# Kernel optimization log

Hardware: AMD Instinct MI355X
Metric: run time of the kernel (lower is better)

The kernel has to match this reference:

```python
import jax, jax.numpy as jnp
import numpy as np

HEADS = 20
HEAD_DIM = 64
NUM_TOKENS = 4


def _split_heads(x, B):
    # (B, S, H*D) -> (B, H, S, D)
    return x.reshape(B, -1, HEADS, HEAD_DIM).transpose(0, 2, 1, 3)


def setup_inputs() -> dict:
    key = jax.random.key(0)
    ks = jax.random.split(key, 10)
    B, HW, hid, cad, Ltxt = 2, 4096, 1280, 2048, 77
    w = lambda k, shp: (jax.random.normal(k, shp, jnp.float32) * 0.02)
    return {
        "hidden_states": jax.random.normal(ks[0], (B, HW, hid), jnp.float32),
        "encoder_hidden_states": jax.random.normal(ks[1], (B, Ltxt + NUM_TOKENS, cad), jnp.float32),
        "indices_to_alter": jax.random.randint(ks[2], (B,), 0, Ltxt, jnp.int32),
        "Wq": w(ks[3], (hid, hid)),
        "Wk": w(ks[4], (cad, hid)),
        "Wv": w(ks[5], (cad, hid)),
        "Wk_nest": w(ks[6], (cad, hid)),
        "Wv_nest": w(ks[7], (cad, hid)),
        "Wout": w(ks[8], (hid, hid)),
        "b_out": jnp.zeros((hid,), jnp.float32),
    }


def reference(hidden_states, encoder_hidden_states, indices_to_alter,
              Wq, Wk, Wv, Wk_nest, Wv_nest, Wout, b_out):
    B, HW, _ = hidden_states.shape
    end = encoder_hidden_states.shape[1] - NUM_TOKENS
    txt = encoder_hidden_states[:, :end]   # (B, Ltxt, cad)
    img = encoder_hidden_states[:, end:]   # (B, num_tokens, cad)

    q = _split_heads(hidden_states @ Wq, B)   # (B, H, HW, D)
    k = _split_heads(txt @ Wk, B)             # (B, H, Lt, D)
    v = _split_heads(txt @ Wv, B)             # (B, H, Lt, D)
    kn = _split_heads(img @ Wk_nest, B)       # (B, H, T, D)
    vn = _split_heads(img @ Wv_nest, B)       # (B, H, T, D)

    sc = 1.0 / jnp.sqrt(jnp.float32(HEAD_DIM))

    # nested attention: per-spatial-position identity value V* (SDPA over image tokens)
    wn = jax.nn.softmax(jnp.einsum('bhqd,bhkd->bhqk', q, kn) * sc, axis=-1)
    value_id = jnp.einsum('bhqk,bhkd->bhqd', wn, vn)          # (B, H, HW, D)

    # main cross attention over text tokens
    w = jax.nn.softmax(jnp.einsum('bhqd,bhkd->bhqk', q, k) * sc, axis=-1)  # (B,H,HW,Lt)
    base = jnp.einsum('bhqk,bhkd->bhqd', w, v)                # (B, H, HW, D)

    # V_mixed[b,h,i] differs from value only at text slot s_b, where it equals value_id[b,h,i].
    # sum_k w[...,k] * V_mixed[...,k,:] == w @ v + w[...,s]*(value_id - v[:, :, s])
    s = indices_to_alter
    w_s = jnp.take_along_axis(w, s[:, None, None, None], axis=3)   # (B, H, HW, 1)
    v_s = jnp.take_along_axis(v, s[:, None, None, None], axis=2)   # (B, H, 1, D)
    out = base + w_s * (value_id - v_s)                             # (B, H, HW, D)

    out = out.transpose(0, 2, 1, 3).reshape(B, HW, HEADS * HEAD_DIM)
    return out @ Wout + b_out
```

## Files before the change

### kernel.cpp

```cpp
#include <hip/hip_runtime.h>
#include <hip/hip_bf16.h>


typedef unsigned short ushort_t;
typedef __attribute__((ext_vector_type(8))) short short8;
typedef __attribute__((ext_vector_type(4))) float f32x4;

#define B_   2
#define HW_  4096
#define HID_ 1280
#define CAD_ 2048
#define LTXT 77
#define NTOK 4
#define NH_  20
#define HD_  64

__device__ __forceinline__ ushort_t f2bf(float f) {
    __hip_bfloat16 h = __float2bfloat16(f);
    return *reinterpret_cast<ushort_t*>(&h);
}

__device__ __forceinline__ void gld_lds16(const void* g, void* l) {
    __builtin_amdgcn_global_load_lds(
        (const __attribute__((address_space(1))) unsigned int*)g,
        (__attribute__((address_space(3))) unsigned int*)l,
        16, 0, 0);
}

__global__ __launch_bounds__(256) void prep(
    const float* __restrict__ hs, const float* __restrict__ enc,
    const float* __restrict__ s0, const float* __restrict__ s1,
    const float* __restrict__ s2, const float* __restrict__ s3,
    const float* __restrict__ s4, const float* __restrict__ s5,
    ushort_t* __restrict__ hsb, ushort_t* __restrict__ encb,
    ushort_t* __restrict__ d0, ushort_t* __restrict__ d1,
    ushort_t* __restrict__ d2, ushort_t* __restrict__ d3,
    ushort_t* __restrict__ d4, ushort_t* __restrict__ d5)
{
    const int y = blockIdx.y, t = threadIdx.x;
    if (y <= 1) {
        const float* src = y ? enc : hs;
        ushort_t* dst = y ? encb : hsb;
        int n4 = y ? (B_ * (LTXT + NTOK) * CAD_) / 4 : (B_ * HW_ * HID_) / 4;
        int step = gridDim.x * 256;
        for (int i = blockIdx.x * 256 + t; i < n4; i += step) {
            float4 v = *(const float4*)(src + (size_t)i * 4);
            ushort_t o[4] = { f2bf(v.x), f2bf(v.y), f2bf(v.z), f2bf(v.w) };
            *(uint2*)(dst + (size_t)i * 4) = *(uint2*)o;
        }
        return;
    }
    int z = y - 2;
    const float* S; ushort_t* D; int K_;
    switch (z) {
        case 0: S = s0; D = d0; K_ = 1280; break;
        case 1: S = s1; D = d1; K_ = 2048; break;
        case 2: S = s2; D = d2; K_ = 2048; break;
        case 3: S = s3; D = d3; K_ = 2048; break;
        case 4: S = s4; D = d4; K_ = 2048; break;
        default: S = s5; D = d5; K_ = 1280; break;
    }
    int tr = blockIdx.x / 40, tc = blockIdx.x % 40;
    if (tr >= K_ / 32) return;
    __shared__ ushort_t tl[32][33];
    int c = t & 31, r0 = t >> 5;
#pragma unroll
    for (int i = 0; i < 4; i++) {
        int r = r0 + i * 8;
        tl[r][c] = f2bf(S[(size_t)(tr * 32 + r) * 1280 + tc * 32 + c]);
    }
    __syncthreads();
#pragma unroll
    for (int i = 0; i < 4; i++) {
        int r = r0 + i * 8;
        D[(size_t)(tc * 32 + r) * K_ + tr * 32 + c] = tl[c][r];
    }
}

template <bool F32OUT>
__device__ __forceinline__ void gemm_body(
    const ushort_t* __restrict__ A, const ushort_t* __restrict__ Bt,
    void* __restrict__ Cout, const float* __restrict__ biasf,
    int M, int K, int lda, int row0, int col0)
{
    __shared__ ushort_t lsA[2][128 * 32];
    __shared__ ushort_t lsB[2][128 * 32];
    const int t = threadIdx.x;
    const int w = t >> 6, l = t & 63;
    const int mb = (w >> 1) * 64, nb = (w & 1) * 64;
    const int lrow = l & 15, lk = (l >> 4) * 8;

    const int r0s = t >> 2, cs = (t & 3) * 8;
    int ra0 = row0 + r0s;       if (ra0 > M - 1) ra0 = M - 1;
    int ra1 = row0 + r0s + 64;  if (ra1 > M - 1) ra1 = M - 1;
    const ushort_t* gA0 = A + (size_t)ra0 * lda + cs;
    const ushort_t* gA1 = A + (size_t)ra1 * lda + cs;
    const ushort_t* gB0 = Bt + (size_t)(col0 + r0s) * K + cs;
    const ushort_t* gB1 = Bt + (size_t)(col0 + r0s + 64) * K + cs;

#define STAGE_(bf, k0) do { \
        gld_lds16(gA0 + (k0), &lsA[bf][(size_t)t * 8]); \
        gld_lds16(gA1 + (k0), &lsA[bf][(size_t)(256 + t) * 8]); \
        gld_lds16(gB0 + (k0), &lsB[bf][(size_t)t * 8]); \
        gld_lds16(gB1 + (k0), &lsB[bf][(size_t)(256 + t) * 8]); \
    } while (0)

    f32x4 acc[4][4] = {};
    STAGE_(0, 0);
    __syncthreads();
    int cur = 0;
    for (int k0 = 0; k0 < K; k0 += 32) {
        if (k0 + 32 < K) STAGE_(cur ^ 1, k0 + 32);
        short8 af[4], bfr[4];
#pragma unroll
        for (int mt = 0; mt < 4; mt++)
            af[mt] = *(const short8*)&lsA[cur][(mb + mt * 16 + lrow) * 32 + lk];
#pragma unroll
        for (int nt = 0; nt < 4; nt++)
            bfr[nt] = *(const short8*)&lsB[cur][(nb + nt * 16 + lrow) * 32 + lk];
#pragma unroll
        for (int mt = 0; mt < 4; mt++)
#pragma unroll
            for (int nt = 0; nt < 4; nt++)
                acc[mt][nt] = __builtin_amdgcn_mfma_f32_16x16x32_bf16(
                    af[mt], bfr[nt], acc[mt][nt], 0, 0, 0);
        __syncthreads();
        cur ^= 1;
    }
#undef STAGE_

    const int quad = l >> 4, cl = l & 15;
#pragma unroll
    for (int nt = 0; nt < 4; nt++) {
        int col = col0 + nb + nt * 16 + cl;
        float bv = biasf ? biasf[col] : 0.f;
#pragma unroll
        for (int mt = 0; mt < 4; mt++)
#pragma unroll
            for (int r = 0; r < 4; r++) {
                int row = row0 + mb + mt * 16 + quad * 4 + r;
                if (row < M) {
                    if (F32OUT)
                        ((float*)Cout)[(size_t)row * 1280 + col] = acc[mt][nt][r] + bv;
                    else
                        ((ushort_t*)Cout)[(size_t)row * 1280 + col] = f2bf(acc[mt][nt][r] + bv);
                }
            }
    }
}

__global__ __launch_bounds__(256, 4) void gemm_q_kv(
    const ushort_t* __restrict__ hsb, const ushort_t* __restrict__ encb,
    const ushort_t* __restrict__ WqT,
    const ushort_t* __restrict__ WkT, const ushort_t* __restrict__ WvT,
    const ushort_t* __restrict__ WknT, const ushort_t* __restrict__ WvnT,
    ushort_t* __restrict__ qb, ushort_t* __restrict__ kb, ushort_t* __restrict__ vb,
    ushort_t* __restrict__ knb, ushort_t* __restrict__ vnb)
{
    int x = blockIdx.x, col0 = blockIdx.y * 128;
    if (x < 64) {
        gemm_body<false>(hsb, WqT, qb, nullptr, B_ * HW_, HID_, HID_, x * 128, col0);
        return;
    }
    int z = x - 64, kind = z & 1;
    const ushort_t* A; const ushort_t* Bt; ushort_t* C; int M;
    if (z < 4) {
        int bb = z >> 1;
        M = LTXT;
        A = encb + (size_t)bb * (LTXT + NTOK) * CAD_;
        Bt = kind ? WvT : WkT;
        C = (kind ? vb : kb) + (size_t)bb * LTXT * HID_;
    } else {
        int bb = (z - 4) >> 1;
        M = NTOK;
        A = encb + ((size_t)bb * (LTXT + NTOK) + LTXT) * CAD_;
        Bt = kind ? WvnT : WknT;
        C = (kind ? vnb : knb) + (size_t)bb * NTOK * HID_;
    }
    gemm_body<false>(A, Bt, C, nullptr, M, CAD_, CAD_, 0, col0);
}

__global__ __launch_bounds__(256, 4) void gemm_bt_f32(
    const ushort_t* __restrict__ A, const ushort_t* __restrict__ Bt,
    float* __restrict__ C, const float* __restrict__ biasf, int M, int K, int lda)
{
    gemm_body<true>(A, Bt, C, biasf, M, K, lda, blockIdx.x * 128, blockIdx.y * 128);
}

__global__ __launch_bounds__(256, 3) void attn_kernel(
    const ushort_t* __restrict__ qb, const ushort_t* __restrict__ kbf,
    const ushort_t* __restrict__ vbf, const ushort_t* __restrict__ knb,
    const ushort_t* __restrict__ vnb, const int* __restrict__ sidx,
    ushort_t* __restrict__ ob)
{
    const int qt = blockIdx.x, h = blockIdx.y, b = blockIdx.z;
    const int t = threadIdx.x, w = t >> 6, l = t & 63;
    const int s_idx = sidx[b];
    __shared__ ushort_t Kl[96 * 72];
    __shared__ ushort_t VT[64 * 104];
    __shared__ ushort_t QP[128 * 104];

    for (int id = t; id < 96 * 8; id += 256) {
        int key = id >> 3, c = (id & 7) * 8;
        uint4 v;
        if (key < LTXT)
            v = *(const uint4*)&kbf[((size_t)(b * LTXT + key)) * HID_ + h * HD_ + c];
        else if (key >= 80 && key < 80 + NTOK)
            v = *(const uint4*)&knb[((size_t)(b * NTOK + key - 80)) * HID_ + h * HD_ + c];
        else
            v = make_uint4(0u, 0u, 0u, 0u);
        *(uint4*)&Kl[key * 72 + c] = v;
    }
    for (int c8 = (t >> 7); c8 < 8; c8 += 2) {
        int key = t & 127;
        if (key < 96) {
            uint4 v = make_uint4(0u, 0u, 0u, 0u);
            if (key < LTXT)
                v = *(const uint4*)&vbf[((size_t)(b * LTXT + key)) * HID_ + h * HD_ + c8 * 8];
            else if (key >= 80 && key < 80 + NTOK)
                v = *(const uint4*)&vnb[((size_t)(b * NTOK + key - 80)) * HID_ + h * HD_ + c8 * 8];
            ushort_t tmp[8];
            *(uint4*)tmp = v;
#pragma unroll
            for (int j = 0; j < 8; j++)
                VT[(c8 * 8 + j) * 104 + key] = tmp[j];
        }
    }
    const int q0 = qt * 128;
    for (int id = t; id < 128 * 8; id += 256) {
        int r = id >> 3, c = (id & 7) * 8;
        uint4 v = *(const uint4*)&qb[((size_t)(b * HW_ + q0 + r)) * HID_ + h * HD_ + c];
        *(uint4*)&QP[r * 72 + c] = v;
    }
    __syncthreads();

    const int mbw = w * 32, lrow = l & 15, lk = (l >> 4) * 8;
    const int quad = l >> 4, cl = l & 15;

    f32x4 S[2][6] = {};
#pragma unroll
    for (int ks = 0; ks < 2; ks++) {
        short8 af0 = *(const short8*)&QP[(mbw + lrow) * 72 + ks * 32 + lk];
        short8 af1 = *(const short8*)&QP[(mbw + 16 + lrow) * 72 + ks * 32 + lk];
#pragma unroll
        for (int nt = 0; nt < 6; nt++) {
            short8 bf = *(const short8*)&Kl[(nt * 16 + lrow) * 72 + ks * 32 + lk];
            S[0][nt] = __builtin_amdgcn_mfma_f32_16x16x32_bf16(af0, bf, S[0][nt], 0, 0, 0);
            S[1][nt] = __builtin_amdgcn_mfma_f32_16x16x32_bf16(af1, bf, S[1][nt], 0, 0, 0);
        }
    }
    __syncthreads();

    const float sc = 0.125f;
#pragma unroll
    for (int mt = 0; mt < 2; mt++) {
#pragma unroll
        for (int r = 0; r < 4; r++) {
            float v[6];
#pragma unroll
            for (int nt = 0; nt < 6; nt++) v[nt] = S[mt][nt][r] * sc;
            float m = -1e30f;
#pragma unroll
            for (int nt = 0; nt < 5; nt++) {
                int c = nt * 16 + cl;
                if (c < LTXT) m = fmaxf(m, v[nt]);
            }
#pragma unroll
            for (int off = 1; off < 16; off <<= 1) m = fmaxf(m, __shfl_xor(m, off));
            float e[5], lsum = 0.f, wsn = 0.f;
#pragma unroll
            for (int nt = 0; nt < 5; nt++) {
                int c = nt * 16 + cl;
                float ev = (c < LTXT) ? __expf(v[nt] - m) : 0.f;
                e[nt] = ev; lsum += ev;
                if (c == s_idx) wsn += ev;
            }
#pragma unroll
            for (int off = 1; off < 16; off <<= 1) {
                lsum += __shfl_xor(lsum, off);
                wsn  += __shfl_xor(wsn, off);
            }
            float inv = 1.f / lsum;
            float ws = wsn * inv;
            bool nv = (cl < 4);
            float m5 = nv ? v[5] : -1e30f;
#pragma unroll
            for (int off = 1; off < 16; off <<= 1) m5 = fmaxf(m5, __shfl_xor(m5, off));
            float e5 = nv ? __expf(v[5] - m5) : 0.f;
            float l5 = e5;
#pragma unroll
            for (int off = 1; off < 16; off <<= 1) l5 += __shfl_xor(l5, off);
            float p5 = ws * e5 / l5;
            int row = mbw + mt * 16 + quad * 4 + r;
#pragma unroll
            for (int nt = 0; nt < 5; nt++) {
                int c = nt * 16 + cl;
                float p = (c < LTXT && c != s_idx) ? e[nt] * inv : 0.f;
                QP[row * 104 + c] = f2bf(p);
            }
            QP[row * 104 + 80 + cl] = f2bf(p5);
        }
    }
    __syncthreads();

    f32x4 O[2][4] = {};
#pragma unroll
    for (int ks = 0; ks < 3; ks++) {
        short8 af0 = *(const short8*)&QP[(mbw + lrow) * 104 + ks * 32 + lk];
        short8 af1 = *(const short8*)&QP[(mbw + 16 + lrow) * 104 + ks * 32 + lk];
#pragma unroll
        for (int nt = 0; nt < 4; nt++) {
            short8 bf = *(const short8*)&VT[(nt * 16 + lrow) * 104 + ks * 32 + lk];
            O[0][nt] = __builtin_amdgcn_mfma_f32_16x16x32_bf16(af0, bf, O[0][nt], 0, 0, 0);
            O[1][nt] = __builtin_amdgcn_mfma_f32_16x16x32_bf16(af1, bf, O[1][nt], 0, 0, 0);
        }
    }
#pragma unroll
    for (int mt = 0; mt < 2; mt++)
#pragma unroll
        for (int nt = 0; nt < 4; nt++)
#pragma unroll
            for (int r = 0; r < 4; r++) {
                int row = mbw + mt * 16 + quad * 4 + r;
                int d = nt * 16 + cl;
                ob[((size_t)(b * HW_ + q0 + row)) * HID_ + h * HD_ + d] = f2bf(O[mt][nt][r]);
            }
}

extern "C" void kernel_launch(void* const* d_in, const int* in_sizes, int n_in,
                              void* d_out, int out_size, void* d_ws, size_t ws_size,
                              hipStream_t stream) {
    const float* hs   = (const float*)d_in[0];
    const float* enc  = (const float*)d_in[1];
    const int*   idx  = (const int*)d_in[2];
    const float* Wq   = (const float*)d_in[3];
    const float* Wk   = (const float*)d_in[4];
    const float* Wv   = (const float*)d_in[5];
    const float* Wkn  = (const float*)d_in[6];
    const float* Wvn  = (const float*)d_in[7];
    const float* Wout = (const float*)d_in[8];
    const float* bout = (const float*)d_in[9];
    float* out = (float*)d_out;

    ushort_t* ws = (ushort_t*)d_ws;
    size_t o = 0;
    ushort_t* WqT   = ws + o; o += (size_t)1280 * 1280;
    ushort_t* WkT   = ws + o; o += (size_t)1280 * 2048;
    ushort_t* WvT   = ws + o; o += (size_t)1280 * 2048;
    ushort_t* WknT  = ws + o; o += (size_t)1280 * 2048;
    ushort_t* WvnT  = ws + o; o += (size_t)1280 * 2048;
    ushort_t* WoutT = ws + o; o += (size_t)1280 * 1280;
    ushort_t* hsb   = ws + o; o += (size_t)B_ * HW_ * HID_;
    ushort_t* encb  = ws + o; o += (size_t)B_ * (LTXT + NTOK) * CAD_;
    ushort_t* qbuf  = ws + o; o += (size_t)B_ * HW_ * HID_;
    ushort_t* kbuf  = ws + o; o += (size_t)B_ * LTXT * HID_;
    ushort_t* vbuf  = ws + o; o += (size_t)B_ * LTXT * HID_;
    ushort_t* knbuf = ws + o; o += (size_t)B_ * NTOK * HID_;
    ushort_t* vnbuf = ws + o; o += (size_t)B_ * NTOK * HID_;
    ushort_t* attnb = hsb;

    prep<<<dim3(2560, 8), 256, 0, stream>>>(hs, enc, Wq, Wk, Wv, Wkn, Wvn, Wout,
                                            hsb, encb,
                                            WqT, WkT, WvT, WknT, WvnT, WoutT);
    gemm_q_kv<<<dim3(72, 10), 256, 0, stream>>>(hsb, encb, WqT, WkT, WvT, WknT, WvnT,
                                                qbuf, kbuf, vbuf, knbuf, vnbuf);
    attn_kernel<<<dim3(HW_ / 128, NH_, B_), 256, 0, stream>>>(qbuf, kbuf, vbuf,
                                                              knbuf, vnbuf, idx, attnb);
    gemm_bt_f32<<<dim3(64, 10), 256, 0, stream>>>(attnb, WoutT, out, bout,
                                                  B_ * HW_, HID_, HID_);
}
```

Measured before the change: 276.9 us.

## Triple-buffer GEMM LDS pipeline with one barrier per k-step

Switches the GEMM mainloop from double to triple buffering, so global-to-LDS loads are issued two steps ahead. Each step now waits with vmcnt(4) and a single barrier instead of a full sync after compute. This hides more load latency and drops one barrier per iteration. In exchange, LDS use grows from 32KB to 48KB per block and launch bounds drop to 3 blocks per CU, which may lower occupancy.

Result: faster. 269.8 us (-2.6%).

```diff
diff --git a/kernel.cpp b/kernel.cpp
--- a/kernel.cpp
+++ b/kernel.cpp
@@ -83,8 +83,8 @@
     void* __restrict__ Cout, const float* __restrict__ biasf,
     int M, int K, int lda, int row0, int col0)
 {
-    __shared__ ushort_t lsA[2][128 * 32];
-    __shared__ ushort_t lsB[2][128 * 32];
+    __shared__ ushort_t lsA[3][128 * 32];
+    __shared__ ushort_t lsB[3][128 * 32];
     const int t = threadIdx.x;
     const int w = t >> 6, l = t & 63;
     const int mb = (w >> 1) * 64, nb = (w & 1) * 64;
@@ -105,28 +105,47 @@
         gld_lds16(gB1 + (k0), &lsB[bf][(size_t)(256 + t) * 8]); \
     } while (0)
 
+#define COMPUTE_(bf) do { \
+        short8 af[4], bfr[4]; \
+        _Pragma("unroll") \
+        for (int mt = 0; mt < 4; mt++) \
+            af[mt] = *(const short8*)&lsA[bf][(mb + mt * 16 + lrow) * 32 + lk]; \
+        _Pragma("unroll") \
+        for (int nt = 0; nt < 4; nt++) \
+            bfr[nt] = *(const short8*)&lsB[bf][(nb + nt * 16 + lrow) * 32 + lk]; \
+        _Pragma("unroll") \
+        for (int mt = 0; mt < 4; mt++) \
+            _Pragma("unroll") \
+            for (int nt = 0; nt < 4; nt++) \
+                acc[mt][nt] = __builtin_amdgcn_mfma_f32_16x16x32_bf16( \
+                    af[mt], bfr[nt], acc[mt][nt], 0, 0, 0); \
+    } while (0)
+
+    const int nsteps = K / 32;
     f32x4 acc[4][4] = {};
+
     STAGE_(0, 0);
-    __syncthreads();
-    int cur = 0;
-    for (int k0 = 0; k0 < K; k0 += 32) {
-        if (k0 + 32 < K) STAGE_(cur ^ 1, k0 + 32);
-        short8 af[4], bfr[4];
-#pragma unroll
-        for (int mt = 0; mt < 4; mt++)
-            af[mt] = *(const short8*)&lsA[cur][(mb + mt * 16 + lrow) * 32 + lk];
-#pragma unroll
-        for (int nt = 0; nt < 4; nt++)
-            bfr[nt] = *(const short8*)&lsB[cur][(nb + nt * 16 + lrow) * 32 + lk];
-#pragma unroll
-        for (int mt = 0; mt < 4; mt++)
-#pragma unroll
-            for (int nt = 0; nt < 4; nt++)
-                acc[mt][nt] = __builtin_amdgcn_mfma_f32_16x16x32_bf16(
-                    af[mt], bfr[nt], acc[mt][nt], 0, 0, 0);
-        __syncthreads();
-        cur ^= 1;
-    }
+    STAGE_(1, 32);
+
+    int bsel = 0;
+    for (int ts = 0; ts < nsteps - 1; ++ts) {
+        asm volatile("s_waitcnt vmcnt(4)" ::: "memory");
+        __builtin_amdgcn_s_barrier();
+        asm volatile("" ::: "memory");
+        COMPUTE_(bsel);
+        int nx = ts + 2;
+        if (nx < nsteps) {
+            int nbuf = bsel + 2; if (nbuf >= 3) nbuf -= 3;
+            STAGE_(nbuf, nx * 32);
+        }
+        bsel = bsel + 1; if (bsel >= 3) bsel -= 3;
+    }
+    asm volatile("s_waitcnt vmcnt(0)" ::: "memory");
+    __builtin_amdgcn_s_barrier();
+    asm volatile("" ::: "memory");
+    COMPUTE_(bsel);
+
+#undef COMPUTE_
 #undef STAGE_
 
     const int quad = l >> 4, cl = l & 15;
@@ -149,7 +168,7 @@
     }
 }
 
-__global__ __launch_bounds__(256, 4) void gemm_q_kv(
+__global__ __launch_bounds__(256, 3) void gemm_q_kv(
     const ushort_t* __restrict__ hsb, const ushort_t* __restrict__ encb,
     const ushort_t* __restrict__ WqT,
     const ushort_t* __restrict__ WkT, const ushort_t* __restrict__ WvT,
@@ -180,7 +199,7 @@
     gemm_body<false>(A, Bt, C, nullptr, M, CAD_, CAD_, 0, col0);
 }
 
-__global__ __launch_bounds__(256, 4) void gemm_bt_f32(
+__global__ __launch_bounds__(256, 3) void gemm_bt_f32(
     const ushort_t* __restrict__ A, const ushort_t* __restrict__ Bt,
     float* __restrict__ C, const float* __restrict__ biasf, int M, int K, int lda)
 {
```

## Load GEMM fragments directly from global into registers, dropping LDS staging

Applied to the files above, without the earlier changes.

The GEMM body stops staging A/B tiles in shared memory via global_load_lds with double buffering and barriers. Each lane now loads its MFMA fragments straight from global memory into registers, using a two-deep register prefetch across K steps of 32. Occupancy hints drop from 4 to 3 blocks to make room for the extra registers. This removes LDS traffic and __syncthreads, but each tile element is now fetched from global/L2 by both waves that share it, and the 16-byte per-lane loads are strided by rows, so coalescing is worse.

New measurement: 430.7 us. 55.6% more time.

```diff
diff --git a/kernel.cpp b/kernel.cpp
--- a/kernel.cpp
+++ b/kernel.cpp
@@ -18,13 +18,6 @@
 __device__ __forceinline__ ushort_t f2bf(float f) {
     __hip_bfloat16 h = __float2bfloat16(f);
     return *reinterpret_cast<ushort_t*>(&h);
-}
-
-__device__ __forceinline__ void gld_lds16(const void* g, void* l) {
-    __builtin_amdgcn_global_load_lds(
-        (const __attribute__((address_space(1))) unsigned int*)g,
-        (__attribute__((address_space(3))) unsigned int*)l,
-        16, 0, 0);
 }
 
 __global__ __launch_bounds__(256) void prep(
@@ -83,51 +76,60 @@
     void* __restrict__ Cout, const float* __restrict__ biasf,
     int M, int K, int lda, int row0, int col0)
 {
-    __shared__ ushort_t lsA[2][128 * 32];
-    __shared__ ushort_t lsB[2][128 * 32];
     const int t = threadIdx.x;
     const int w = t >> 6, l = t & 63;
     const int mb = (w >> 1) * 64, nb = (w & 1) * 64;
     const int lrow = l & 15, lk = (l >> 4) * 8;
 
-    const int r0s = t >> 2, cs = (t & 3) * 8;
-    int ra0 = row0 + r0s;       if (ra0 > M - 1) ra0 = M - 1;
-    int ra1 = row0 + r0s + 64;  if (ra1 > M - 1) ra1 = M - 1;
-    const ushort_t* gA0 = A + (size_t)ra0 * lda + cs;
-    const ushort_t* gA1 = A + (size_t)ra1 * lda + cs;
-    const ushort_t* gB0 = Bt + (size_t)(col0 + r0s) * K + cs;
-    const ushort_t* gB1 = Bt + (size_t)(col0 + r0s + 64) * K + cs;
-
-#define STAGE_(bf, k0) do { \
-        gld_lds16(gA0 + (k0), &lsA[bf][(size_t)t * 8]); \
-        gld_lds16(gA1 + (k0), &lsA[bf][(size_t)(256 + t) * 8]); \
-        gld_lds16(gB0 + (k0), &lsB[bf][(size_t)t * 8]); \
-        gld_lds16(gB1 + (k0), &lsB[bf][(size_t)(256 + t) * 8]); \
-    } while (0)
+    const ushort_t* pA[4];
+    const ushort_t* pB[4];
+#pragma unroll
+    for (int mt = 0; mt < 4; mt++) {
+        int r = row0 + mb + mt * 16 + lrow;
+        if (r > M - 1) r = M - 1;
+        pA[mt] = A + (size_t)r * lda + lk;
+    }
+#pragma unroll
+    for (int nt = 0; nt < 4; nt++) {
+        int c = col0 + nb + nt * 16 + lrow;
+        pB[nt] = Bt + (size_t)c * K + lk;
+    }
 
     f32x4 acc[4][4] = {};
-    STAGE_(0, 0);
-    __syncthreads();
-    int cur = 0;
-    for (int k0 = 0; k0 < K; k0 += 32) {
-        if (k0 + 32 < K) STAGE_(cur ^ 1, k0 + 32);
-        short8 af[4], bfr[4];
-#pragma unroll
-        for (int mt = 0; mt < 4; mt++)
-            af[mt] = *(const short8*)&lsA[cur][(mb + mt * 16 + lrow) * 32 + lk];
-#pragma unroll
-        for (int nt = 0; nt < 4; nt++)
-            bfr[nt] = *(const short8*)&lsB[cur][(nb + nt * 16 + lrow) * 32 + lk];
+    short8 a0[4], b0[4], a1[4], b1[4];
+
+#pragma unroll
+    for (int i = 0; i < 4; i++) {
+        a0[i] = *(const short8*)(pA[i]);
+        b0[i] = *(const short8*)(pB[i]);
+    }
+
+    for (int k0 = 0; k0 < K; k0 += 64) {
+#pragma unroll
+        for (int i = 0; i < 4; i++) {
+            a1[i] = *(const short8*)(pA[i] + k0 + 32);
+            b1[i] = *(const short8*)(pB[i] + k0 + 32);
+        }
 #pragma unroll
         for (int mt = 0; mt < 4; mt++)
 #pragma unroll
             for (int nt = 0; nt < 4; nt++)
                 acc[mt][nt] = __builtin_amdgcn_mfma_f32_16x16x32_bf16(
-                    af[mt], bfr[nt], acc[mt][nt], 0, 0, 0);
-        __syncthreads();
-        cur ^= 1;
-    }
-#undef STAGE_
+                    a0[mt], b0[nt], acc[mt][nt], 0, 0, 0);
+        if (k0 + 64 < K) {
+#pragma unroll
+            for (int i = 0; i < 4; i++) {
+                a0[i] = *(const short8*)(pA[i] + k0 + 64);
+                b0[i] = *(const short8*)(pB[i] + k0 + 64);
+            }
+        }
+#pragma unroll
+        for (int mt = 0; mt < 4; mt++)
+#pragma unroll
+            for (int nt = 0; nt < 4; nt++)
+                acc[mt][nt] = __builtin_amdgcn_mfma_f32_16x16x32_bf16(
+                    a1[mt], b1[nt], acc[mt][nt], 0, 0, 0);
+    }
 
     const int quad = l >> 4, cl = l & 15;
 #pragma unroll
@@ -149,7 +151,7 @@
     }
 }
 
-__global__ __launch_bounds__(256, 4) void gemm_q_kv(
+__global__ __launch_bounds__(256, 3) void gemm_q_kv(
     const ushort_t* __restrict__ hsb, const ushort_t* __restrict__ encb,
     const ushort_t* __restrict__ WqT,
     const ushort_t* __restrict__ WkT, const ushort_t* __restrict__ WvT,
@@ -180,7 +182,7 @@
     gemm_body<false>(A, Bt, C, nullptr, M, CAD_, CAD_, 0, col0);
 }
 
-__global__ __launch_bounds__(256, 4) void gemm_bt_f32(
+__global__ __launch_bounds__(256, 3) void gemm_bt_f32(
     const ushort_t* __restrict__ A, const ushort_t* __restrict__ Bt,
     float* __restrict__ C, const float* __restrict__ biasf, int M, int K, int lda)
 {
```
